# Kernel tuning notes

Hardware: AMD Instinct MI355X
Metric: run time of the kernel (lower is better)

The kernel has to match this reference:

```python
import jax, jax.numpy as jnp
import numpy as np

GAMMA = 1.0  # weight on CRL loss
BETA = 1.0   # weight on MDCA calibration loss
B, C = 4096, 32000
DATASET_SIZE = 50000


def setup_inputs() -> dict:
    key = jax.random.key(0)
    k1, k2, k3, k4 = jax.random.split(key, 4)
    logits = jax.random.normal(k1, (B, C), dtype=jnp.float32)
    targets = jax.random.randint(k2, (B,), 0, C, dtype=jnp.int64)
    idx = jax.random.randint(k3, (B,), 0, DATASET_SIZE, dtype=jnp.int64)
    # normalized historical correctness per dataset sample (History table)
    correctness = jax.random.uniform(k4, (DATASET_SIZE,), dtype=jnp.float32)
    return {"logits": logits, "targets": targets, "idx": idx, "correctness": correctness}


def reference(logits, targets, idx, correctness):
    b, c = logits.shape
    logp = jax.nn.log_softmax(logits, axis=1)
    # CrossEntropyLoss (mean reduction)
    loss_cls = -jnp.mean(jnp.take_along_axis(logp, targets[:, None], axis=1))
    p = jnp.exp(logp)  # softmax probabilities, reused by MDCA and CRL

    # MDCA: mean_c | mean_b p[:, c] - freq(target == c) |, fused (no per-class loop)
    avg_conf = jnp.mean(p, axis=0)                                  # [C]
    avg_count = jnp.zeros((c,), logits.dtype).at[targets].add(1.0) / b  # [C]
    loss_cal = jnp.mean(jnp.abs(avg_conf - avg_count))

    # CRL (rank_target='softmax'): max-softmax confidence margin ranking
    conf = jnp.max(p, axis=1)          # [B]
    conf2 = jnp.roll(conf, -1)
    idx2 = jnp.roll(idx, -1)
    c1 = correctness[idx]
    c2 = correctness[idx2]
    rank_target = jnp.sign(c1 - c2)                     # {-1, 0, +1}
    rank_margin = jnp.abs(c1 - c2)
    tnz = jnp.where(rank_target == 0, jnp.ones_like(rank_target), rank_target)
    rank_input2 = conf2 + rank_margin / tnz
    # MarginRankingLoss(margin=0, mean): mean(max(0, -target*(x1 - x2)))
    loss_ref = jnp.mean(jnp.maximum(0.0, -rank_target * (conf - rank_input2)))

    return loss_cls + GAMMA * loss_ref + BETA * loss_cal
```

## Files before the change

kernel.cpp:

```cpp
#include <hip/hip_runtime.h>
#include <math.h>


__global__ __launch_bounds__(256) void pass1_kernel(
    const float* __restrict__ logits, const int* __restrict__ targets,
    float* __restrict__ rowm, float* __restrict__ rowinv,
    float* __restrict__ celogp, float* __restrict__ counts, int C)
{
    const int b   = blockIdx.x;
    const int tid = threadIdx.x;
    const float* row = logits + (size_t)b * (size_t)C;

    float m = -INFINITY, s = 0.0f;
    const int n4 = C >> 2;
    const float4* row4 = (const float4*)row;
    for (int i = tid; i < n4; i += 256) {
        float4 v = row4[i];
        float vm = fmaxf(fmaxf(v.x, v.y), fmaxf(v.z, v.w));
        float nm = fmaxf(m, vm);
        s = s * __expf(m - nm)
          + __expf(v.x - nm) + __expf(v.y - nm)
          + __expf(v.z - nm) + __expf(v.w - nm);
        m = nm;
    }
    for (int i = (n4 << 2) + tid; i < C; i += 256) {
        float v = row[i];
        float nm = fmaxf(m, v);
        s = s * __expf(m - nm) + __expf(v - nm);
        m = nm;
    }

    for (int off = 32; off; off >>= 1) {
        float om = __shfl_down(m, off, 64);
        float os = __shfl_down(s, off, 64);
        float nm = fmaxf(m, om);
        s = s * __expf(m - nm) + os * __expf(om - nm);
        m = nm;
    }
    __shared__ float sm[4], ss[4];
    const int wid = tid >> 6, lane = tid & 63;
    if (lane == 0) { sm[wid] = m; ss[wid] = s; }
    __syncthreads();
    if (tid == 0) {
        m = sm[0]; s = ss[0];
        #pragma unroll
        for (int w = 1; w < 4; ++w) {
            float om = sm[w], os = ss[w];
            float nm = fmaxf(m, om);
            s = s * __expf(m - nm) + os * __expf(om - nm);
            m = nm;
        }
        rowm[b]   = m;
        rowinv[b] = 1.0f / s;
        int t = targets[b];
        celogp[b] = row[t] - m - logf(s);
        atomicAdd(&counts[t], 1.0f);
    }
}

#define RPG 64
__global__ __launch_bounds__(256) void pass2_kernel(
    const float* __restrict__ logits, const float* __restrict__ rowm,
    const float* __restrict__ rowinv, float* __restrict__ colsum,
    int B, int C)
{
    const int tid  = threadIdx.x;
    const int base = blockIdx.x * 2048;
    const int ncols = min(2048, C - base);
    const int c0 = base + (tid << 2);
    const int c1 = base + 1024 + (tid << 2);
    const bool v0 = (tid << 2) < ncols;
    const bool v1 = (1024 + (tid << 2)) < ncols;

    __shared__ float smem_m[RPG], smem_i[RPG];
    const int r0 = blockIdx.y * RPG;
    const int nr = min(RPG, B - r0);
    if (tid < nr) { smem_m[tid] = rowm[r0 + tid]; smem_i[tid] = rowinv[r0 + tid]; }
    __syncthreads();

    float4 a0 = make_float4(0.f, 0.f, 0.f, 0.f);
    float4 a1 = make_float4(0.f, 0.f, 0.f, 0.f);
    #pragma unroll 4
    for (int r = 0; r < nr; ++r) {
        const float mm = smem_m[r];
        const float iv = smem_i[r];
        const float* row = logits + (size_t)(r0 + r) * (size_t)C;
        if (v0) {
            float4 v = *(const float4*)(row + c0);
            a0.x += __expf(v.x - mm) * iv;
            a0.y += __expf(v.y - mm) * iv;
            a0.z += __expf(v.z - mm) * iv;
            a0.w += __expf(v.w - mm) * iv;
        }
        if (v1) {
            float4 v = *(const float4*)(row + c1);
            a1.x += __expf(v.x - mm) * iv;
            a1.y += __expf(v.y - mm) * iv;
            a1.z += __expf(v.z - mm) * iv;
            a1.w += __expf(v.w - mm) * iv;
        }
    }
    if (v0) {
        atomicAdd(&colsum[c0 + 0], a0.x);
        atomicAdd(&colsum[c0 + 1], a0.y);
        atomicAdd(&colsum[c0 + 2], a0.z);
        atomicAdd(&colsum[c0 + 3], a0.w);
    }
    if (v1) {
        atomicAdd(&colsum[c1 + 0], a1.x);
        atomicAdd(&colsum[c1 + 1], a1.y);
        atomicAdd(&colsum[c1 + 2], a1.z);
        atomicAdd(&colsum[c1 + 3], a1.w);
    }
}

__global__ __launch_bounds__(1024) void final_kernel(
    const float* __restrict__ rowinv, const float* __restrict__ celogp,
    const int* __restrict__ idx, const int* __restrict__ targets_unused,
    const float* __restrict__ correctness,
    const float* __restrict__ colsum, const float* __restrict__ counts,
    float* __restrict__ out, int B, int C)
{
    const int tid = threadIdx.x;
    float sum_ce = 0.f, sum_crl = 0.f, sum_cal = 0.f;

    for (int b = tid; b < B; b += 1024) {
        sum_ce += celogp[b];
        const int b2 = (b + 1 == B) ? 0 : b + 1;
        const float conf  = rowinv[b];
        const float conf2 = rowinv[b2];
        const float c1 = correctness[idx[b]];
        const float c2 = correctness[idx[b2]];
        const float rt  = (c1 > c2) ? 1.f : ((c1 < c2) ? -1.f : 0.f);
        const float rm  = fabsf(c1 - c2);
        const float tnz = (rt == 0.f) ? 1.f : rt;
        const float ri2 = conf2 + rm / tnz;
        sum_crl += fmaxf(0.f, -rt * (conf - ri2));
    }
    for (int c = tid; c < C; c += 1024) {
        sum_cal += fabsf(colsum[c] - counts[c]);
    }

    for (int off = 32; off; off >>= 1) {
        sum_ce  += __shfl_down(sum_ce,  off, 64);
        sum_crl += __shfl_down(sum_crl, off, 64);
        sum_cal += __shfl_down(sum_cal, off, 64);
    }
    __shared__ float red[3][16];
    const int wid = tid >> 6, lane = tid & 63;
    if (lane == 0) { red[0][wid] = sum_ce; red[1][wid] = sum_crl; red[2][wid] = sum_cal; }
    __syncthreads();
    if (tid == 0) {
        float tce = 0.f, tcrl = 0.f, tcal = 0.f;
        #pragma unroll
        for (int w = 0; w < 16; ++w) { tce += red[0][w]; tcrl += red[1][w]; tcal += red[2][w]; }
        const float loss_cls = -tce / (float)B;
        const float loss_ref = tcrl / (float)B;
        const float loss_cal = tcal / ((float)B * (float)C);
        out[0] = loss_cls + loss_ref + loss_cal;
    }
}

extern "C" void kernel_launch(void* const* d_in, const int* in_sizes, int n_in,
                              void* d_out, int out_size, void* d_ws, size_t ws_size,
                              hipStream_t stream) {
    const float* logits      = (const float*)d_in[0];
    const int*   targets     = (const int*)d_in[1];
    const int*   idx         = (const int*)d_in[2];
    const float* correctness = (const float*)d_in[3];
    float* out = (float*)d_out;

    const int B = in_sizes[1];
    const int C = in_sizes[0] / B;

    char* ws = (char*)d_ws;
    float* rowm   = (float*)ws;                      ws += (size_t)B * sizeof(float);
    float* rowinv = (float*)ws;                      ws += (size_t)B * sizeof(float);
    float* celogp = (float*)ws;                      ws += (size_t)B * sizeof(float);
    float* colsum = (float*)ws;                      ws += (size_t)C * sizeof(float);
    float* counts = (float*)ws;

    hipMemsetAsync(colsum, 0, (size_t)C * sizeof(float), stream);
    hipMemsetAsync(counts, 0, (size_t)C * sizeof(float), stream);

    pass1_kernel<<<B, 256, 0, stream>>>(logits, targets, rowm, rowinv, celogp, counts, C);

    dim3 g2((C + 2047) / 2048, (B + RPG - 1) / RPG);
    pass2_kernel<<<g2, 256, 0, stream>>>(logits, rowm, rowinv, colsum, B, C);

    final_kernel<<<1, 1024, 0, stream>>>(rowinv, celogp, idx, targets, correctness,
                                         colsum, counts, out, B, C);
}
```

Baseline: 807.8 us.

## Cache exp values as fp8 in pass one and column-sum from the fp8 copy

The row-statistics kernel now loads each row once into registers using 1024 threads. It computes the max and the exp-sum in two reductions instead of an online softmax. It also writes exp(x-m) scaled by 256 as packed fp8 to a workspace buffer. The column-sum kernel then reads this quarter-size fp8 buffer instead of re-reading the fp32 logits and recomputing the exponentials, which cuts the second full pass over the input. In exchange, the calibration term's column sums carry fp8 quantisation error. Tail handling for C values not divisible by 4 or 16 is also dropped.

```diff
diff --git a/kernel.cpp b/kernel.cpp
--- a/kernel.cpp
+++ b/kernel.cpp
@@ -2,122 +2,121 @@
 #include <math.h>
 
 
-__global__ __launch_bounds__(256) void pass1_kernel(
+#define TPB_A 1024
+#define NV 8
+
+__global__ __launch_bounds__(TPB_A) void rowstat_pack_kernel(
     const float* __restrict__ logits, const int* __restrict__ targets,
-    float* __restrict__ rowm, float* __restrict__ rowinv,
-    float* __restrict__ celogp, float* __restrict__ counts, int C)
+    unsigned int* __restrict__ q8,
+    float* __restrict__ rowinv, float* __restrict__ celogp,
+    float* __restrict__ counts, int C)
 {
-    const int b   = blockIdx.x;
-    const int tid = threadIdx.x;
-    const float* row = logits + (size_t)b * (size_t)C;
+    const int b = blockIdx.x, tid = threadIdx.x;
+    const int n4 = C >> 2;
+    const float4* row4 = (const float4*)(logits + (size_t)b * (size_t)C);
+    unsigned int* out = q8 + (size_t)b * (size_t)n4;
 
-    float m = -INFINITY, s = 0.0f;
-    const int n4 = C >> 2;
-    const float4* row4 = (const float4*)row;
-    for (int i = tid; i < n4; i += 256) {
-        float4 v = row4[i];
-        float vm = fmaxf(fmaxf(v.x, v.y), fmaxf(v.z, v.w));
-        float nm = fmaxf(m, vm);
-        s = s * __expf(m - nm)
-          + __expf(v.x - nm) + __expf(v.y - nm)
-          + __expf(v.z - nm) + __expf(v.w - nm);
-        m = nm;
-    }
-    for (int i = (n4 << 2) + tid; i < C; i += 256) {
-        float v = row[i];
-        float nm = fmaxf(m, v);
-        s = s * __expf(m - nm) + __expf(v - nm);
-        m = nm;
+    float4 f[NV];
+    float lm = -1e30f;
+    #pragma unroll
+    for (int j = 0; j < NV; ++j) {
+        const int i = tid + TPB_A * j;
+        f[j] = (i < n4) ? row4[i] : make_float4(-1e30f, -1e30f, -1e30f, -1e30f);
+        lm = fmaxf(lm, fmaxf(fmaxf(f[j].x, f[j].y), fmaxf(f[j].z, f[j].w)));
     }
 
-    for (int off = 32; off; off >>= 1) {
-        float om = __shfl_down(m, off, 64);
-        float os = __shfl_down(s, off, 64);
-        float nm = fmaxf(m, om);
-        s = s * __expf(m - nm) + os * __expf(om - nm);
-        m = nm;
+    for (int off = 32; off; off >>= 1) lm = fmaxf(lm, __shfl_xor(lm, off, 64));
+    __shared__ float redm[TPB_A / 64];
+    __shared__ float reds[TPB_A / 64];
+    const int wid = tid >> 6;
+    if ((tid & 63) == 0) redm[wid] = lm;
+    __syncthreads();
+    float m = redm[0];
+    #pragma unroll
+    for (int w = 1; w < TPB_A / 64; ++w) m = fmaxf(m, redm[w]);
+
+    float ls = 0.f;
+    #pragma unroll
+    for (int j = 0; j < NV; ++j) {
+        const float e0 = __expf(f[j].x - m);
+        const float e1 = __expf(f[j].y - m);
+        const float e2 = __expf(f[j].z - m);
+        const float e3 = __expf(f[j].w - m);
+        const int i = tid + TPB_A * j;
+        if (i < n4) {
+            ls += (e0 + e1) + (e2 + e3);
+            int pk = __builtin_amdgcn_cvt_pk_fp8_f32(e0 * 256.f, e1 * 256.f, 0, false);
+            pk     = __builtin_amdgcn_cvt_pk_fp8_f32(e2 * 256.f, e3 * 256.f, pk, true);
+            out[i] = (unsigned int)pk;
+        }
     }
-    __shared__ float sm[4], ss[4];
-    const int wid = tid >> 6, lane = tid & 63;
-    if (lane == 0) { sm[wid] = m; ss[wid] = s; }
+
+    for (int off = 32; off; off >>= 1) ls += __shfl_xor(ls, off, 64);
+    if ((tid & 63) == 0) reds[wid] = ls;
     __syncthreads();
     if (tid == 0) {
-        m = sm[0]; s = ss[0];
+        float s = 0.f;
         #pragma unroll
-        for (int w = 1; w < 4; ++w) {
-            float om = sm[w], os = ss[w];
-            float nm = fmaxf(m, om);
-            s = s * __expf(m - nm) + os * __expf(om - nm);
-            m = nm;
-        }
-        rowm[b]   = m;
+        for (int w = 0; w < TPB_A / 64; ++w) s += reds[w];
         rowinv[b] = 1.0f / s;
-        int t = targets[b];
-        celogp[b] = row[t] - m - logf(s);
+        const int t = targets[b];
+        celogp[b] = logits[(size_t)b * (size_t)C + t] - m - logf(s);
         atomicAdd(&counts[t], 1.0f);
     }
 }
 
 #define RPG 64
-__global__ __launch_bounds__(256) void pass2_kernel(
-    const float* __restrict__ logits, const float* __restrict__ rowm,
-    const float* __restrict__ rowinv, float* __restrict__ colsum,
-    int B, int C)
+__global__ __launch_bounds__(256) void colsum_fp8_kernel(
+    const unsigned int* __restrict__ q8, const float* __restrict__ rowinv,
+    float* __restrict__ colsum, int B, int C)
 {
-    const int tid  = threadIdx.x;
-    const int base = blockIdx.x * 2048;
-    const int ncols = min(2048, C - base);
-    const int c0 = base + (tid << 2);
-    const int c1 = base + 1024 + (tid << 2);
-    const bool v0 = (tid << 2) < ncols;
-    const bool v1 = (1024 + (tid << 2)) < ncols;
-
-    __shared__ float smem_m[RPG], smem_i[RPG];
+    const int n4 = C >> 2;
+    const int tid = threadIdx.x;
+    const int dbase = blockIdx.x * 1024 + (tid << 2);
     const int r0 = blockIdx.y * RPG;
     const int nr = min(RPG, B - r0);
-    if (tid < nr) { smem_m[tid] = rowm[r0 + tid]; smem_i[tid] = rowinv[r0 + tid]; }
+
+    __shared__ float sinv[RPG];
+    if (tid < nr) sinv[tid] = rowinv[r0 + tid];
     __syncthreads();
 
-    float4 a0 = make_float4(0.f, 0.f, 0.f, 0.f);
-    float4 a1 = make_float4(0.f, 0.f, 0.f, 0.f);
-    #pragma unroll 4
+    if (dbase + 4 > n4) return;
+
+    float acc[16];
+    #pragma unroll
+    for (int i = 0; i < 16; ++i) acc[i] = 0.f;
+
+    #pragma unroll 2
     for (int r = 0; r < nr; ++r) {
-        const float mm = smem_m[r];
-        const float iv = smem_i[r];
-        const float* row = logits + (size_t)(r0 + r) * (size_t)C;
-        if (v0) {
-            float4 v = *(const float4*)(row + c0);
-            a0.x += __expf(v.x - mm) * iv;
-            a0.y += __expf(v.y - mm) * iv;
-            a0.z += __expf(v.z - mm) * iv;
-            a0.w += __expf(v.w - mm) * iv;
-        }
-        if (v1) {
-            float4 v = *(const float4*)(row + c1);
-            a1.x += __expf(v.x - mm) * iv;
-            a1.y += __expf(v.y - mm) * iv;
-            a1.z += __expf(v.z - mm) * iv;
-            a1.w += __expf(v.w - mm) * iv;
-        }
+        const float inv = sinv[r];
+        const uint4 v = *(const uint4*)(q8 + (size_t)(r0 + r) * (size_t)n4 + dbase);
+        acc[0]  += __builtin_amdgcn_cvt_f32_fp8(v.x, 0) * inv;
+        acc[1]  += __builtin_amdgcn_cvt_f32_fp8(v.x, 1) * inv;
+        acc[2]  += __builtin_amdgcn_cvt_f32_fp8(v.x, 2) * inv;
+        acc[3]  += __builtin_amdgcn_cvt_f32_fp8(v.x, 3) * inv;
+        acc[4]  += __builtin_amdgcn_cvt_f32_fp8(v.y, 0) * inv;
+        acc[5]  += __builtin_amdgcn_cvt_f32_fp8(v.y, 1) * inv;
+        acc[6]  += __builtin_amdgcn_cvt_f32_fp8(v.y, 2) * inv;
+        acc[7]  += __builtin_amdgcn_cvt_f32_fp8(v.y, 3) * inv;
+        acc[8]  += __builtin_amdgcn_cvt_f32_fp8(v.z, 0) * inv;
+        acc[9]  += __builtin_amdgcn_cvt_f32_fp8(v.z, 1) * inv;
+        acc[10] += __builtin_amdgcn_cvt_f32_fp8(v.z, 2) * inv;
+        acc[11] += __builtin_amdgcn_cvt_f32_fp8(v.z, 3) * inv;
+        acc[12] += __builtin_amdgcn_cvt_f32_fp8(v.w, 0) * inv;
+        acc[13] += __builtin_amdgcn_cvt_f32_fp8(v.w, 1) * inv;
+        acc[14] += __builtin_amdgcn_cvt_f32_fp8(v.w, 2) * inv;
+        acc[15] += __builtin_amdgcn_cvt_f32_fp8(v.w, 3) * inv;
     }
-    if (v0) {
-        atomicAdd(&colsum[c0 + 0], a0.x);
-        atomicAdd(&colsum[c0 + 1], a0.y);
-        atomicAdd(&colsum[c0 + 2], a0.z);
-        atomicAdd(&colsum[c0 + 3], a0.w);
-    }
-    if (v1) {
-        atomicAdd(&colsum[c1 + 0], a1.x);
-        atomicAdd(&colsum[c1 + 1], a1.y);
-        atomicAdd(&colsum[c1 + 2], a1.z);
-        atomicAdd(&colsum[c1 + 3], a1.w);
-    }
+
+    const int c0 = dbase << 2;
+    const float sc = 1.0f / 256.0f;
+    #pragma unroll
+    for (int i = 0; i < 16; ++i) atomicAdd(&colsum[c0 + i], acc[i] * sc);
 }
 
-__global__ __launch_bounds__(1024) void final_kernel(
+__global__ __launch_bounds__(1024) void final_loss_kernel(
     const float* __restrict__ rowinv, const float* __restrict__ celogp,
-    const int* __restrict__ idx, const int* __restrict__ targets_unused,
-    const float* __restrict__ correctness,
+    const int* __restrict__ idx, const float* __restrict__ correctness,
     const float* __restrict__ colsum, const float* __restrict__ counts,
     float* __restrict__ out, int B, int C)
 {
@@ -172,9 +171,10 @@
 
     const int B = in_sizes[1];
     const int C = in_sizes[0] / B;
+    const int n4 = C >> 2;
 
     char* ws = (char*)d_ws;
-    float* rowm   = (float*)ws;                      ws += (size_t)B * sizeof(float);
+    unsigned int* q8 = (unsigned int*)ws;            ws += (size_t)B * (size_t)n4 * 4;
     float* rowinv = (float*)ws;                      ws += (size_t)B * sizeof(float);
     float* celogp = (float*)ws;                      ws += (size_t)B * sizeof(float);
     float* colsum = (float*)ws;                      ws += (size_t)C * sizeof(float);
@@ -183,11 +183,12 @@
     hipMemsetAsync(colsum, 0, (size_t)C * sizeof(float), stream);
     hipMemsetAsync(counts, 0, (size_t)C * sizeof(float), stream);
 
-    pass1_kernel<<<B, 256, 0, stream>>>(logits, targets, rowm, rowinv, celogp, counts, C);
+    rowstat_pack_kernel<<<B, TPB_A, 0, stream>>>(logits, targets, q8,
+                                                 rowinv, celogp, counts, C);
 
-    dim3 g2((C + 2047) / 2048, (B + RPG - 1) / RPG);
-    pass2_kernel<<<g2, 256, 0, stream>>>(logits, rowm, rowinv, colsum, B, C);
+    dim3 g2((n4 + 1023) / 1024, (B + RPG - 1) / RPG);
+    colsum_fp8_kernel<<<g2, 256, 0, stream>>>(q8, rowinv, colsum, B, C);
 
-    final_kernel<<<1, 1024, 0, stream>>>(rowinv, celogp, idx, targets, correctness,
-                                         colsum, counts, out, B, C);
+    final_loss_kernel<<<1, 1024, 0, stream>>>(rowinv, celogp, idx, correctness,
+                                              colsum, counts, out, B, C);
 }
```

Result: slower. 844.4 us (+4.5%).
